# Kernel optimization log

Measured on AMD Instinct MI355X. Metric: run time of the kernel, lower is better.

## Reference

```python
import jax, jax.numpy as jnp
import numpy as np
import math

N, E, C, H = 16384, 8192, 256, 8
NNZ = 262144  # incidence pairs, avg vertex degree 16


def setup_inputs() -> dict:
    key = jax.random.key(0)
    ks = jax.random.split(key, 12)
    s = 1.0 / math.sqrt(C)
    inp = {
        "X": jax.random.normal(ks[0], (N, C), dtype=jnp.float32),
        "v_ids": jax.random.randint(ks[1], (NNZ,), 0, N, dtype=jnp.int32),
        "e_ids": jax.random.randint(ks[2], (NNZ,), 0, E, dtype=jnp.int32),
        # Linear params stored as [in, out]; y = x @ W + b  (matches torch x @ W.T + b)
        "Wq": jax.random.uniform(ks[3], (C, C), jnp.float32, -s, s),
        "bq": jax.random.uniform(ks[4], (C,), jnp.float32, -s, s),
        "Wk": jax.random.uniform(ks[5], (C, C), jnp.float32, -s, s),
        "bk": jax.random.uniform(ks[6], (C,), jnp.float32, -s, s),
        "Wv": jax.random.uniform(ks[7], (C, C), jnp.float32, -s, s),
        "bv": jax.random.uniform(ks[8], (C,), jnp.float32, -s, s),
        "Wke": jax.random.uniform(ks[9], (C, C), jnp.float32, -s, s),
        "bke": jax.random.uniform(ks[10], (C,), jnp.float32, -s, s),
    }
    return inp


def reference(X, v_ids, e_ids, Wq, bq, Wk, bk, Wv, bv, Wke, bke):
    d = C // H
    scale = 1.0 / math.sqrt(d)

    Q = (X @ Wq + bq).reshape(N, H, d)
    K = (X @ Wk + bk).reshape(N, H, d)
    V = (X @ Wv + bv).reshape(N, H, d)

    # hg.v2e_aggregation(X, 'mean'): segment-mean of incident vertex features per hyperedge
    sums = jax.ops.segment_sum(X[v_ids], e_ids, num_segments=E)          # [E, C]
    cnt = jax.ops.segment_sum(jnp.ones((NNZ,), X.dtype), e_ids, num_segments=E)
    Xe = sums / jnp.maximum(cnt, 1.0)[:, None]                            # [E, C]

    Ke = Xe @ Wke + bke                                                   # [E, C]
    Qe = X @ Wq + bq                                                      # [N, C]

    # per-node attention over heads: [N, H, H]
    attn_n = jax.nn.softmax(jnp.einsum('nhd,ngd->nhg', Q, K) * scale, axis=-1)
    X_node = jnp.einsum('nhg,ngd->nhd', attn_n, V).reshape(N, C)          # [N, C]

    # node -> hyperedge attention: [N, E]
    attn_e = jax.nn.softmax((Qe @ Ke.T) * scale, axis=-1)
    X_hyperedge = attn_e @ Xe                                             # [N, C]

    out = X_node + X_hyperedge
    # is_last=False: ReLU; bn=None; dropout in eval mode (identity)
    return jax.nn.relu(out)
```

## Files before the change

### kernel.cpp

```cpp
#include <hip/hip_runtime.h>

typedef unsigned short u16;
typedef unsigned int u32;
typedef __attribute__((ext_vector_type(4))) float f32x4;
typedef __attribute__((ext_vector_type(16))) float f32x16;
typedef __attribute__((ext_vector_type(8))) short bf16x8;
typedef __attribute__((ext_vector_type(4))) short bf16x4;
typedef __attribute__((ext_vector_type(4))) u16 u16x4;
typedef __attribute__((ext_vector_type(2))) u32 u32x2;
typedef __attribute__((ext_vector_type(4))) u32 u32x4;

#define N_NODES 16384
#define N_EDGES 8192
#define FK_SCALE 0.17677669529663687f
#define LOG2E 1.4426950408889634f
#define C1EXP (FK_SCALE * LOG2E)

typedef const u32 __attribute__((address_space(1))) gu32;
typedef u32 __attribute__((address_space(3))) lu32;

__device__ __forceinline__ void gl_lds16(const void* g, void* l) {
  __builtin_amdgcn_global_load_lds((gu32*)g, (lu32*)l, 16, 0, 0);
}

__device__ __forceinline__ float b2f(u16 u) {
  return __builtin_bit_cast(float, (u32)u << 16);
}
__device__ __forceinline__ u16 f2b(float f) {
  u32 u = __builtin_bit_cast(u32, f);
  u += 0x7fffu + ((u >> 16) & 1u);
  return (u16)(u >> 16);
}

__device__ __forceinline__ u32 cvtpk(float a, float b) {
  u32 r;
  asm("v_cvt_pk_bf16_f32 %0, %1, %2" : "=v"(r) : "v"(a), "v"(b));
  return r;
}

__device__ __forceinline__ u32x2 swap32v(u32 x, u32 y) {
#if __has_builtin(__builtin_amdgcn_permlane32_swap)
  auto r = __builtin_amdgcn_permlane32_swap(x, y, false, false);
  u32x2 out = {(u32)r[0], (u32)r[1]};
  return out;
#else
  u32 px = __shfl_xor(x, 32, 64), py = __shfl_xor(y, 32, 64);
  bool hi = (threadIdx.x & 32) != 0;
  u32x2 out = {hi ? x : py, hi ? px : y};
  return out;
#endif
}

__global__ __launch_bounds__(256) void k_prep(const float* __restrict__ X,
                                              const int* __restrict__ e_ids,
                                              u16* __restrict__ Xb,
                                              int* __restrict__ hist,
                                              const float* __restrict__ Wq,
                                              const float* __restrict__ Wk,
                                              const float* __restrict__ Wv,
                                              const float* __restrict__ Wke,
                                              const float* __restrict__ bq,
                                              const float* __restrict__ bk,
                                              const float* __restrict__ bv,
                                              const float* __restrict__ bke,
                                              u16* __restrict__ Wt,
                                              float* __restrict__ bcat) {
  __shared__ float tile[64][65];
  int b = blockIdx.x;
  int tid = threadIdx.x;
  if (b < 4096) {
    int i = b * 256 + tid;
    f32x4 v = *(const f32x4*)(X + (size_t)i * 4);
    u16x4 r;
    r.x = f2b(v.x); r.y = f2b(v.y); r.z = f2b(v.z); r.w = f2b(v.w);
    *(u16x4*)(Xb + (size_t)i * 4) = r;
    if (tid < 64) atomicAdd(&hist[e_ids[b * 64 + tid]], 1);
    return;
  }
  int local = b - 4096;
  int w = local >> 4, rem = local & 15;
  int k0 = (rem >> 2) * 64, n0 = (rem & 3) * 64;
  const float* W = (w == 0) ? Wq : (w == 1) ? Wk : (w == 2) ? Wv : Wke;
  if (rem == 0) {
    const float* bb = (w == 0) ? bq : (w == 1) ? bk : (w == 2) ? bv : bke;
    bcat[w * 256 + tid] = bb[tid];
  }
#pragma unroll
  for (int i = 0; i < 16; i++) {
    int idx = i * 256 + tid;
    int kr = idx >> 6, nc = idx & 63;
    tile[nc][kr] = W[(k0 + kr) * 256 + n0 + nc];
  }
  __syncthreads();
#pragma unroll
  for (int i = 0; i < 16; i++) {
    int idx = i * 256 + tid;
    int nr = idx >> 6, kc = idx & 63;
    Wt[w * 65536 + (n0 + nr) * 256 + k0 + kc] = f2b(tile[nr][kc]);
  }
}

__global__ __launch_bounds__(256) void k_scan(const int* __restrict__ hist,
                                              int* __restrict__ eoff,
                                              int* __restrict__ cur) {
  __shared__ int ts[256];
  int t = threadIdx.x;
  int base = t * 32;
  int vals[32];
  int s = 0;
#pragma unroll
  for (int i = 0; i < 32; i++) { vals[i] = hist[base + i]; s += vals[i]; }
  ts[t] = s;
  __syncthreads();
  for (int off = 1; off < 256; off <<= 1) {
    int v = (t >= off) ? ts[t - off] : 0;
    __syncthreads();
    ts[t] += v;
    __syncthreads();
  }
  int ex = ts[t] - s;
#pragma unroll
  for (int i = 0; i < 32; i++) {
    eoff[base + i] = ex;
    cur[base + i] = ex;
    ex += vals[i];
  }
  if (t == 255) eoff[8192] = ex;
}

__global__ __launch_bounds__(256) void k_perm(const int* __restrict__ v_ids,
                                              const int* __restrict__ e_ids,
                                              int* __restrict__ cur,
                                              int* __restrict__ perm) {
  int base = blockIdx.x * 1024 + threadIdx.x;
#pragma unroll
  for (int k = 0; k < 4; k++) {
    int i = base + k * 256;
    int e = e_ids[i];
    int v = v_ids[i];
    int pos = atomicAdd(&cur[e], 1);
    perm[pos] = v;
  }
}

__global__ __launch_bounds__(256) void k_gg(const u16* __restrict__ Xb,
                                            const int* __restrict__ perm,
                                            const int* __restrict__ eoff,
                                            u16* __restrict__ Xe,
                                            u16* __restrict__ XeTc,
                                            const u16* __restrict__ Wt,
                                            const float* __restrict__ bcat,
                                            u16* __restrict__ QKV) {
  __shared__ u16 As[128 * 64];
  __shared__ u16 Bs[128 * 64];
  int b = blockIdx.x;
  int tid = threadIdx.x;
  int wave = tid >> 6, lane = tid & 63;
  if (b < 768) {
    int quad = lane >> 4, l16 = lane & 15;
    int wm = wave >> 1, wn = wave & 1;
    int mtile = (b & 127) * 128, ntile = (b >> 7) * 128;
    const u16* Ap = Xb + (size_t)mtile * 256;
    const u16* Bp = Wt + (size_t)ntile * 256;
    f32x4 acc[4][4];
#pragma unroll
    for (int am = 0; am < 4; am++)
#pragma unroll
      for (int bn = 0; bn < 4; bn++) acc[am][bn] = (f32x4){0.f, 0.f, 0.f, 0.f};
    for (int ks = 0; ks < 4; ks++) {
      __syncthreads();
#pragma unroll
      for (int i = 0; i < 4; i++) {
        int s = i * 256 + tid;
        int r = s >> 3, c = s & 7;
        gl_lds16(Ap + r * 256 + ks * 64 + ((c ^ (r & 7)) << 3), As + s * 8);
      }
#pragma unroll
      for (int i = 0; i < 4; i++) {
        int s = i * 256 + tid;
        int r = s >> 3, c = s & 7;
        gl_lds16(Bp + r * 256 + ks * 64 + ((c ^ (r & 7)) << 3), Bs + s * 8);
      }
      __syncthreads();
#pragma unroll
      for (int kc = 0; kc < 2; kc++) {
        bf16x8 a[4], bb[4];
        int cc = kc * 4 + quad;
#pragma unroll
        for (int am = 0; am < 4; am++) {
          int rl = wm * 64 + am * 16 + l16;
          a[am] = *(const bf16x8*)(As + rl * 64 + ((cc ^ (rl & 7)) << 3));
        }
#pragma unroll
        for (int bn = 0; bn < 4; bn++) {
          int rl = wn * 64 + bn * 16 + l16;
          bb[bn] = *(const bf16x8*)(Bs + rl * 64 + ((cc ^ (rl & 7)) << 3));
        }
#pragma unroll
        for (int am = 0; am < 4; am++)
#pragma unroll
          for (int bn = 0; bn < 4; bn++)
            acc[am][bn] = __builtin_amdgcn_mfma_f32_16x16x32_bf16(a[am], bb[bn], acc[am][bn], 0, 0, 0);
      }
    }
#pragma unroll
    for (int am = 0; am < 4; am++)
#pragma unroll
      for (int bn = 0; bn < 4; bn++)
#pragma unroll
        for (int r = 0; r < 4; r++) {
          int row = mtile + wm * 64 + am * 16 + quad * 4 + r;
          int col = ntile + wn * 64 + bn * 16 + l16;
          QKV[(size_t)row * 768 + col] = f2b(acc[am][bn][r] + bcat[col]);
        }
    return;
  }
  int e = (b - 768) * 4 + wave;
  int start = eoff[e], end = eoff[e + 1];
  int cnt = end - start;
  int pidx = 0;
  if (lane < cnt) pidx = perm[start + lane];
  f32x4 acc = {0.f, 0.f, 0.f, 0.f};
  int n1 = cnt < 64 ? cnt : 64;
  for (int j = 0; j < n1; j++) {
    int v = __shfl(pidx, j, 64);
    bf16x4 x = *(const bf16x4*)(Xb + (size_t)v * 256 + lane * 4);
#pragma unroll
    for (int c = 0; c < 4; c++) acc[c] += b2f((u16)x[c]);
  }
  for (int j = start + 64; j < end; j++) {
    int v = perm[j];
    bf16x4 x = *(const bf16x4*)(Xb + (size_t)v * 256 + lane * 4);
#pragma unroll
    for (int c = 0; c < 4; c++) acc[c] += b2f((u16)x[c]);
  }
  float inv = 1.0f / fmaxf((float)cnt, 1.0f);
  u16x4 r;
  r.x = f2b(acc.x * inv); r.y = f2b(acc.y * inv);
  r.z = f2b(acc.z * inv); r.w = f2b(acc.w * inv);
  *(u16x4*)(Xe + (size_t)e * 256 + lane * 4) = r;
  size_t tb = (size_t)(e >> 3) * 2048 + (e & 7);
  XeTc[tb + (lane * 4 + 0) * 8] = r.x;
  XeTc[tb + (lane * 4 + 1) * 8] = r.y;
  XeTc[tb + (lane * 4 + 2) * 8] = r.z;
  XeTc[tb + (lane * 4 + 3) * 8] = r.w;
}

__global__ __launch_bounds__(256) void k_gemmke(const u16* __restrict__ A,
                                                const u16* __restrict__ Wt,
                                                const float* __restrict__ bias,
                                                u16* __restrict__ KebT) {
  __shared__ u16 As[128 * 64];
  __shared__ u16 Bs[128 * 64];
  int tid = threadIdx.x;
  int wave = tid >> 6, lane = tid & 63;
  int quad = lane >> 4, l16 = lane & 15;
  int wm = wave >> 1, wn = wave & 1;
  int mtile = blockIdx.x * 128, ntile = blockIdx.y * 128;
  const u16* Ap = A + (size_t)mtile * 256;
  const u16* Bp = Wt + (size_t)ntile * 256;
  f32x4 acc[4][4];
#pragma unroll
  for (int am = 0; am < 4; am++)
#pragma unroll
    for (int bn = 0; bn < 4; bn++) acc[am][bn] = (f32x4){0.f, 0.f, 0.f, 0.f};
  for (int ks = 0; ks < 4; ks++) {
    __syncthreads();
#pragma unroll
    for (int i = 0; i < 4; i++) {
      int s = i * 256 + tid;
      int r = s >> 3, c = s & 7;
      gl_lds16(Ap + r * 256 + ks * 64 + ((c ^ (r & 7)) << 3), As + s * 8);
    }
#pragma unroll
    for (int i = 0; i < 4; i++) {
      int s = i * 256 + tid;
      int r = s >> 3, c = s & 7;
      gl_lds16(Bp + r * 256 + ks * 64 + ((c ^ (r & 7)) << 3), Bs + s * 8);
    }
    __syncthreads();
#pragma unroll
    for (int kc = 0; kc < 2; kc++) {
      bf16x8 a[4], b[4];
      int cc = kc * 4 + quad;
#pragma unroll
      for (int am = 0; am < 4; am++) {
        int rl = wm * 64 + am * 16 + l16;
        a[am] = *(const bf16x8*)(As + rl * 64 + ((cc ^ (rl & 7)) << 3));
      }
#pragma unroll
      for (int bn = 0; bn < 4; bn++) {
        int rl = wn * 64 + bn * 16 + l16;
        b[bn] = *(const bf16x8*)(Bs + rl * 64 + ((cc ^ (rl & 7)) << 3));
      }
#pragma unroll
      for (int am = 0; am < 4; am++)
#pragma unroll
        for (int bn = 0; bn < 4; bn++)
          acc[am][bn] = __builtin_amdgcn_mfma_f32_16x16x32_bf16(a[am], b[bn], acc[am][bn], 0, 0, 0);
    }
  }
#pragma unroll
  for (int am = 0; am < 4; am++)
#pragma unroll
    for (int bn = 0; bn < 4; bn++)
#pragma unroll
      for (int r = 0; r < 4; r++) {
        int row = mtile + wm * 64 + am * 16 + quad * 4 + r;
        int col = ntile + wn * 64 + bn * 16 + l16;
        KebT[(size_t)(col >> 3) * 65536 + row * 8 + (col & 7)] = f2b(acc[am][bn][r] + bias[col]);
      }
}

__device__ __forceinline__ void stage_k(const u16* __restrict__ KebT, u16* KeL,
                                        int kbase, int tid) {
#pragma unroll
  for (int i = 0; i < 4; i++) {
    int s = i * 256 + tid;
    int c = s >> 5, r = s & 31;
    gl_lds16(KebT + ((size_t)c * 8192 + kbase + r) * 8, KeL + s * 8);
  }
}
__device__ __forceinline__ void stage_v(const u16* __restrict__ XeTc, u16* VLT,
                                        int ktg, int tid) {
  int kb8 = ktg * 4;
#pragma unroll
  for (int i = 0; i < 4; i++) {
    int s = i * 256 + tid;
    int kc = s >> 8, ch = s & 255;
    gl_lds16(XeTc + ((size_t)(kb8 + kc) * 256 + ch) * 8, VLT + s * 8);
  }
}

__global__ __launch_bounds__(256, 2) void k_flash(const u16* __restrict__ QKV,
                                                  const u16* __restrict__ KebT,
                                                  const u16* __restrict__ XeTc,
                                                  u16* __restrict__ Op,
                                                  float* __restrict__ Lv) {
  extern __shared__ u16 sm[];
  int tid = threadIdx.x;
  int wave = tid >> 6, lane = tid & 63;
  int l31 = lane & 31, half = lane >> 5;
  int qt = blockIdx.x & 127;
  int split = blockIdx.x >> 7;
  int rowq = qt * 128 + wave * 32 + l31;

  bf16x8 qf[16];
#pragma unroll
  for (int ks = 0; ks < 16; ks++)
    qf[ks] = *(const bf16x8*)(QKV + (size_t)rowq * 768 + ks * 16 + half * 8);

  f32x16 o[8];
#pragma unroll
  for (int i = 0; i < 8; i++)
#pragma unroll
    for (int r = 0; r < 16; r++) o[i][r] = 0.f;
  float lsum = 0.f;

  stage_k(KebT, sm, split * 2048, tid);
  stage_v(XeTc, sm + 8192, split * 64, tid);

#define FLASH_STEP(RB, T)                                                          \
  {                                                                                \
    __syncthreads();            \
    int ktg = split * 64 + (T);                                                    \
    if ((T) + 1 < 64) {                                                            \
      stage_k(KebT, sm + ((RB) ^ 1) * 16384, (ktg + 1) * 32, tid);                 \
      stage_v(XeTc, sm + ((RB) ^ 1) * 16384 + 8192, ktg + 1, tid);                 \
    }                                                                              \
    const u16* kp = sm + (RB) * 16384 + half * 256 + l31 * 8;                      \
    const u16* vp = sm + (RB) * 16384 + 8192 + half * 2048 + l31 * 8;              \
    f32x16 s0;                                                                     \
    _Pragma("unroll") for (int r = 0; r < 16; r++) s0[r] = 0.f;                    \
    __builtin_amdgcn_s_setprio(1);                                                 \
    _Pragma("unroll") for (int ks = 0; ks < 16; ks++) {                            \
      bf16x8 ka = *(const bf16x8*)(kp + ks * 512);                                 \
      s0 = __builtin_amdgcn_mfma_f32_32x32x16_bf16(ka, qf[ks], s0, 0, 0, 0);       \
    }                                                                              \
    __builtin_amdgcn_s_setprio(0);                                                 \
    u32 w[8];                                                                      \
    _Pragma("unroll") for (int i = 0; i < 8; i++) {                                \
      float e0 = __builtin_amdgcn_exp2f(s0[2 * i] * C1EXP);                        \
      float e1 = __builtin_amdgcn_exp2f(s0[2 * i + 1] * C1EXP);                    \
      lsum += e0 + e1;                                                             \
      w[i] = cvtpk(e0, e1);                                                        \
    }                                                                              \
    {                                                                              \
      u32x2 r;                                                                     \
      r = swap32v(w[2], w[0]); w[2] = r.x; w[0] = r.y;                             \
      r = swap32v(w[3], w[1]); w[3] = r.x; w[1] = r.y;                             \
      r = swap32v(w[6], w[4]); w[6] = r.x; w[4] = r.y;                             \
      r = swap32v(w[7], w[5]); w[7] = r.x; w[5] = r.y;                             \
    }                                                                              \
    u32x4 p0v = {w[0], w[1], w[2], w[3]};                                          \
    u32x4 p1v = {w[4], w[5], w[6], w[7]};                                          \
    bf16x8 pf0 = __builtin_bit_cast(bf16x8, p0v);                                  \
    bf16x8 pf1 = __builtin_bit_cast(bf16x8, p1v);                                  \
    __builtin_amdgcn_s_setprio(1);                                                 \
    _Pragma("unroll") for (int ct = 0; ct < 8; ct++) {                             \
      const u16* vpc = vp + ct * 256;                                              \
      o[ct] = __builtin_amdgcn_mfma_f32_32x32x16_bf16(pf0, *(const bf16x8*)(vpc), o[ct], 0, 0, 0); \
      o[ct] = __builtin_amdgcn_mfma_f32_32x32x16_bf16(pf1, *(const bf16x8*)(vpc + 4096), o[ct], 0, 0, 0); \
    }                                                                              \
    __builtin_amdgcn_s_setprio(0);                                                 \
  }

  for (int t2 = 0; t2 < 64; t2 += 2) {
    FLASH_STEP(0, t2);
    FLASH_STEP(1, t2 + 1);
  }
#undef FLASH_STEP

  lsum += __shfl_xor(lsum, 32, 64);
  if (lane < 32) Lv[split * N_NODES + qt * 128 + wave * 32 + l31] = lsum;

  size_t obase = (size_t)split * N_NODES * 256;
#pragma unroll
  for (int ct = 0; ct < 8; ct++)
#pragma unroll
    for (int reg = 0; reg < 16; reg++) {
      int row = qt * 128 + wave * 32 + (reg & 3) + 8 * (reg >> 2) + 4 * half;
      int col = ct * 32 + l31;
      Op[obase + (size_t)row * 256 + col] = f2b(o[ct][reg]);
    }
}

__global__ __launch_bounds__(256) void k_comb(const u16* __restrict__ QKV,
                                              const u16* __restrict__ Op,
                                              const float* __restrict__ Lv,
                                              float* __restrict__ out) {
  int idx = blockIdx.x * 256 + threadIdx.x;
  int n = idx >> 6, lane = idx & 63;
  int h = lane >> 3, g = lane & 7;
  const u16* base = QKV + n * 768;
  const bf16x8* qp = (const bf16x8*)(base + h * 32);
  const bf16x8* kp = (const bf16x8*)(base + 256 + g * 32);
  float s = 0.f;
#pragma unroll
  for (int t = 0; t < 4; t++) {
    bf16x8 qv = qp[t], kv = kp[t];
#pragma unroll
    for (int j = 0; j < 8; j++) s += b2f((u16)qv[j]) * b2f((u16)kv[j]);
  }
  s *= FK_SCALE;
  float mx = s;
#pragma unroll
  for (int off = 1; off < 8; off <<= 1) mx = fmaxf(mx, __shfl_xor(mx, off, 64));
  float p = __builtin_amdgcn_exp2f((s - mx) * LOG2E);
  float lsum = p;
#pragma unroll
  for (int off = 1; off < 8; off <<= 1) lsum += __shfl_xor(lsum, off, 64);
  float attn = p / lsum;
  float a4[4] = {0.f, 0.f, 0.f, 0.f};
#pragma unroll
  for (int g2 = 0; g2 < 8; g2++) {
    float a = __shfl(attn, (lane & 56) | g2, 64);
    bf16x4 vv = *(const bf16x4*)(base + 512 + g2 * 32 + g * 4);
#pragma unroll
    for (int j = 0; j < 4; j++) a4[j] += a * b2f((u16)vv[j]);
  }
  int c4 = lane * 4;
  float L = 0.f;
#pragma unroll
  for (int sl = 0; sl < 4; sl++) L += Lv[sl * N_NODES + n];
  f32x4 acc = {0.f, 0.f, 0.f, 0.f};
#pragma unroll
  for (int sp = 0; sp < 4; sp++) {
    u16x4 ov = *(const u16x4*)(Op + (size_t)sp * N_NODES * 256 + (size_t)n * 256 + c4);
    acc.x += b2f(ov.x);
    acc.y += b2f(ov.y);
    acc.z += b2f(ov.z);
    acc.w += b2f(ov.w);
  }
  float invL = 1.0f / L;
  f32x4 res;
  res.x = fmaxf(acc.x * invL + a4[0], 0.f);
  res.y = fmaxf(acc.y * invL + a4[1], 0.f);
  res.z = fmaxf(acc.z * invL + a4[2], 0.f);
  res.w = fmaxf(acc.w * invL + a4[3], 0.f);
  *(f32x4*)(out + (size_t)n * 256 + c4) = res;
}

extern "C" void kernel_launch(void* const* d_in, const int* in_sizes, int n_in,
                              void* d_out, int out_size, void* d_ws, size_t ws_size,
                              hipStream_t stream) {
  const float* X = (const float*)d_in[0];
  const int* v_ids = (const int*)d_in[1];
  const int* e_ids = (const int*)d_in[2];
  const float* Wq = (const float*)d_in[3];
  const float* bq = (const float*)d_in[4];
  const float* Wk = (const float*)d_in[5];
  const float* bk = (const float*)d_in[6];
  const float* Wv = (const float*)d_in[7];
  const float* bv = (const float*)d_in[8];
  const float* Wke = (const float*)d_in[9];
  const float* bke = (const float*)d_in[10];
  float* out = (float*)d_out;

  char* ws = (char*)d_ws;
  u16* Xb = (u16*)(ws);
  u16* QKV = (u16*)(ws + 8388608);
  u16* Wt = (u16*)(ws + 33554432);
  float* bcat = (float*)(ws + 34078720);
  int* hist = (int*)(ws + 34082816);
  int* eoff = (int*)(ws + 34115584);
  int* cur = (int*)(ws + 34152448);
  int* perm = (int*)(ws + 34185216);
  u16* Xe = (u16*)(ws + 35233792);
  u16* XeTc = (u16*)(ws + 39428096);
  u16* KebT = (u16*)(ws + 43622400);
  u16* Op = (u16*)(ws + 64593920);
  float* Lv = (float*)(ws + 98148352);

  hipMemsetAsync(hist, 0, 32768, stream);
  k_prep<<<4160, 256, 0, stream>>>(X, e_ids, Xb, hist, Wq, Wk, Wv, Wke,
                                   bq, bk, bv, bke, Wt, bcat);
  k_scan<<<1, 256, 0, stream>>>(hist, eoff, cur);
  k_perm<<<256, 256, 0, stream>>>(v_ids, e_ids, cur, perm);
  k_gg<<<2816, 256, 0, stream>>>(Xb, perm, eoff, Xe, XeTc, Wt, bcat, QKV);
  k_gemmke<<<dim3(64, 2), 256, 0, stream>>>(Xe, Wt + 3 * 65536, bcat + 768, KebT);
  hipFuncSetAttribute((const void*)k_flash, hipFuncAttributeMaxDynamicSharedMemorySize,
                      65536);
  k_flash<<<512, 256, 65536, stream>>>(QKV, KebT, XeTc, Op, Lv);
  k_comb<<<4096, 256, 0, stream>>>(QKV, Op, Lv, out);
}
```

Measured before the change: 325.0 us.

## Software-pipeline flash PV with next QK, widen blocks to 512 threads, fold scale into Ke

The flash kernel now runs the P·V MFMAs of the previous tile interleaved with the QK MFMAs of the current tile, using a triple-buffered V region and double-buffered K in LDS. Blocks grow to 512 threads covering 256 query rows, so each staged K/V tile is shared by twice as many waves and the grid is halved. The softmax scale times log2e is folded into the Ke projection output, which removes a multiply per score. This costs more LDS (80KB per block) and register pressure, and may reduce occupancy.

New measurement: 309.0 us (median of 2 runs). -4.9%, faster.

```diff
diff --git a/kernel.cpp b/kernel.cpp
--- a/kernel.cpp
+++ b/kernel.cpp
@@ -308,15 +308,16 @@
       for (int r = 0; r < 4; r++) {
         int row = mtile + wm * 64 + am * 16 + quad * 4 + r;
         int col = ntile + wn * 64 + bn * 16 + l16;
-        KebT[(size_t)(col >> 3) * 65536 + row * 8 + (col & 7)] = f2b(acc[am][bn][r] + bias[col]);
+        KebT[(size_t)(col >> 3) * 65536 + row * 8 + (col & 7)] =
+            f2b((acc[am][bn][r] + bias[col]) * C1EXP);
       }
 }
 
 __device__ __forceinline__ void stage_k(const u16* __restrict__ KebT, u16* KeL,
                                         int kbase, int tid) {
 #pragma unroll
-  for (int i = 0; i < 4; i++) {
-    int s = i * 256 + tid;
+  for (int i = 0; i < 2; i++) {
+    int s = i * 512 + tid;
     int c = s >> 5, r = s & 31;
     gl_lds16(KebT + ((size_t)c * 8192 + kbase + r) * 8, KeL + s * 8);
   }
@@ -325,14 +326,14 @@
                                         int ktg, int tid) {
   int kb8 = ktg * 4;
 #pragma unroll
-  for (int i = 0; i < 4; i++) {
-    int s = i * 256 + tid;
+  for (int i = 0; i < 2; i++) {
+    int s = i * 512 + tid;
     int kc = s >> 8, ch = s & 255;
     gl_lds16(XeTc + ((size_t)(kb8 + kc) * 256 + ch) * 8, VLT + s * 8);
   }
 }
 
-__global__ __launch_bounds__(256, 2) void k_flash(const u16* __restrict__ QKV,
+__global__ __launch_bounds__(512, 2) void k_flash(const u16* __restrict__ QKV,
                                                   const u16* __restrict__ KebT,
                                                   const u16* __restrict__ XeTc,
                                                   u16* __restrict__ Op,
@@ -341,9 +342,9 @@
   int tid = threadIdx.x;
   int wave = tid >> 6, lane = tid & 63;
   int l31 = lane & 31, half = lane >> 5;
-  int qt = blockIdx.x & 127;
-  int split = blockIdx.x >> 7;
-  int rowq = qt * 128 + wave * 32 + l31;
+  int qt = blockIdx.x & 63;
+  int split = blockIdx.x >> 6;
+  int rowq = qt * 256 + wave * 32 + l31;
 
   bf16x8 qf[16];
 #pragma unroll
@@ -356,32 +357,37 @@
 #pragma unroll
     for (int r = 0; r < 16; r++) o[i][r] = 0.f;
   float lsum = 0.f;
+  bf16x8 pf0 = {}, pf1 = {};
 
   stage_k(KebT, sm, split * 2048, tid);
-  stage_v(XeTc, sm + 8192, split * 64, tid);
-
-#define FLASH_STEP(RB, T)                                                          \
+  stage_v(XeTc, sm + 16384, split * 64, tid);
+
+#define FLASH_STEP(T, KB, VR, VW, DO_STAGE, DO_PV)                                 \
   {                                                                                \
-    __syncthreads();            \
-    int ktg = split * 64 + (T);                                                    \
-    if ((T) + 1 < 64) {                                                            \
-      stage_k(KebT, sm + ((RB) ^ 1) * 16384, (ktg + 1) * 32, tid);                 \
-      stage_v(XeTc, sm + ((RB) ^ 1) * 16384 + 8192, ktg + 1, tid);                 \
+    __syncthreads();                                                               \
+    if (DO_STAGE) {                                                                \
+      stage_k(KebT, sm + ((KB) ^ 1) * 8192, (split * 64 + (T) + 1) * 32, tid);     \
+      stage_v(XeTc, sm + 16384 + (VW) * 8192, split * 64 + (T) + 1, tid);          \
     }                                                                              \
-    const u16* kp = sm + (RB) * 16384 + half * 256 + l31 * 8;                      \
-    const u16* vp = sm + (RB) * 16384 + 8192 + half * 2048 + l31 * 8;              \
+    const u16* kp = sm + (KB) * 8192 + half * 256 + l31 * 8;                       \
+    const u16* vp = sm + 16384 + (VR) * 8192 + half * 2048 + l31 * 8;              \
     f32x16 s0;                                                                     \
     _Pragma("unroll") for (int r = 0; r < 16; r++) s0[r] = 0.f;                    \
     __builtin_amdgcn_s_setprio(1);                                                 \
-    _Pragma("unroll") for (int ks = 0; ks < 16; ks++) {                            \
-      bf16x8 ka = *(const bf16x8*)(kp + ks * 512);                                 \
-      s0 = __builtin_amdgcn_mfma_f32_32x32x16_bf16(ka, qf[ks], s0, 0, 0, 0);       \
+    _Pragma("unroll") for (int j = 0; j < 16; j++) {                               \
+      bf16x8 ka = *(const bf16x8*)(kp + j * 512);                                  \
+      s0 = __builtin_amdgcn_mfma_f32_32x32x16_bf16(ka, qf[j], s0, 0, 0, 0);        \
+      if (DO_PV) {                                                                 \
+        bf16x8 vb = *(const bf16x8*)(vp + (j >> 1) * 256 + (j & 1) * 4096);        \
+        o[j >> 1] = __builtin_amdgcn_mfma_f32_32x32x16_bf16(                       \
+            (j & 1) ? pf1 : pf0, vb, o[j >> 1], 0, 0, 0);                          \
+      }                                                                            \
     }                                                                              \
     __builtin_amdgcn_s_setprio(0);                                                 \
     u32 w[8];                                                                      \
     _Pragma("unroll") for (int i = 0; i < 8; i++) {                                \
-      float e0 = __builtin_amdgcn_exp2f(s0[2 * i] * C1EXP);                        \
-      float e1 = __builtin_amdgcn_exp2f(s0[2 * i + 1] * C1EXP);                    \
+      float e0 = __builtin_amdgcn_exp2f(s0[2 * i]);                                \
+      float e1 = __builtin_amdgcn_exp2f(s0[2 * i + 1]);                            \
       lsum += e0 + e1;                                                             \
       w[i] = cvtpk(e0, e1);                                                        \
     }                                                                              \
@@ -394,32 +400,45 @@
     }                                                                              \
     u32x4 p0v = {w[0], w[1], w[2], w[3]};                                          \
     u32x4 p1v = {w[4], w[5], w[6], w[7]};                                          \
-    bf16x8 pf0 = __builtin_bit_cast(bf16x8, p0v);                                  \
-    bf16x8 pf1 = __builtin_bit_cast(bf16x8, p1v);                                  \
-    __builtin_amdgcn_s_setprio(1);                                                 \
-    _Pragma("unroll") for (int ct = 0; ct < 8; ct++) {                             \
-      const u16* vpc = vp + ct * 256;                                              \
-      o[ct] = __builtin_amdgcn_mfma_f32_32x32x16_bf16(pf0, *(const bf16x8*)(vpc), o[ct], 0, 0, 0); \
-      o[ct] = __builtin_amdgcn_mfma_f32_32x32x16_bf16(pf1, *(const bf16x8*)(vpc + 4096), o[ct], 0, 0, 0); \
-    }                                                                              \
-    __builtin_amdgcn_s_setprio(0);                                                 \
-  }
-
-  for (int t2 = 0; t2 < 64; t2 += 2) {
-    FLASH_STEP(0, t2);
-    FLASH_STEP(1, t2 + 1);
-  }
+    pf0 = __builtin_bit_cast(bf16x8, p0v);                                         \
+    pf1 = __builtin_bit_cast(bf16x8, p1v);                                         \
+  }
+
+  FLASH_STEP(0, 0, 0, 1, 1, 0);
+  for (int tb = 1; tb < 61; tb += 6) {
+    FLASH_STEP(tb + 0, 1, 0, 2, 1, 1);
+    FLASH_STEP(tb + 1, 0, 1, 0, 1, 1);
+    FLASH_STEP(tb + 2, 1, 2, 1, 1, 1);
+    FLASH_STEP(tb + 3, 0, 0, 2, 1, 1);
+    FLASH_STEP(tb + 4, 1, 1, 0, 1, 1);
+    FLASH_STEP(tb + 5, 0, 2, 1, 1, 1);
+  }
+  FLASH_STEP(61, 1, 0, 2, 1, 1);
+  FLASH_STEP(62, 0, 1, 0, 1, 1);
+  FLASH_STEP(63, 1, 2, 0, 0, 1);
 #undef FLASH_STEP
 
+  {
+    const u16* vp = sm + 16384 + half * 2048 + l31 * 8;
+    __builtin_amdgcn_s_setprio(1);
+#pragma unroll
+    for (int j = 0; j < 16; j++) {
+      bf16x8 vb = *(const bf16x8*)(vp + (j >> 1) * 256 + (j & 1) * 4096);
+      o[j >> 1] = __builtin_amdgcn_mfma_f32_32x32x16_bf16(
+          (j & 1) ? pf1 : pf0, vb, o[j >> 1], 0, 0, 0);
+    }
+    __builtin_amdgcn_s_setprio(0);
+  }
+
   lsum += __shfl_xor(lsum, 32, 64);
-  if (lane < 32) Lv[split * N_NODES + qt * 128 + wave * 32 + l31] = lsum;
+  if (lane < 32) Lv[split * N_NODES + qt * 256 + wave * 32 + l31] = lsum;
 
   size_t obase = (size_t)split * N_NODES * 256;
 #pragma unroll
   for (int ct = 0; ct < 8; ct++)
 #pragma unroll
     for (int reg = 0; reg < 16; reg++) {
-      int row = qt * 128 + wave * 32 + (reg & 3) + 8 * (reg >> 2) + 4 * half;
+      int row = qt * 256 + wave * 32 + (reg & 3) + 8 * (reg >> 2) + 4 * half;
       int col = ct * 32 + l31;
       Op[obase + (size_t)row * 256 + col] = f2b(o[ct][reg]);
     }
@@ -520,7 +539,7 @@
   k_gg<<<2816, 256, 0, stream>>>(Xb, perm, eoff, Xe, XeTc, Wt, bcat, QKV);
   k_gemmke<<<dim3(64, 2), 256, 0, stream>>>(Xe, Wt + 3 * 65536, bcat + 768, KebT);
   hipFuncSetAttribute((const void*)k_flash, hipFuncAttributeMaxDynamicSharedMemorySize,
-                      65536);
-  k_flash<<<512, 256, 65536, stream>>>(QKV, KebT, XeTc, Op, Lv);
+                      81920);
+  k_flash<<<256, 512, 81920, stream>>>(QKV, KebT, XeTc, Op, Lv);
   k_comb<<<4096, 256, 0, stream>>>(QKV, Op, Lv, out);
 }
```
